# Kernel tuning notes

Measured on AMD Instinct MI355X. Metric: run time of the kernel, lower is better.

The kernel has to match this reference:

```python
import jax, jax.numpy as jnp
import numpy as np

D = 1024
NUM_HEADS = 16
HEAD_DIM = D // NUM_HEADS
INIT_VALUES = 1e-4


def setup_inputs() -> dict:
    key = jax.random.key(0)
    ks = jax.random.split(key, 24)
    s = 0.02
    inp = {
        "v": jax.random.normal(ks[0], (8, 2048, D), dtype=jnp.float32),
        "l": jax.random.normal(ks[1], (8, 512, D), dtype=jnp.float32),
        "ln_v_g": jnp.ones((D,), jnp.float32),
        "ln_v_b": jnp.zeros((D,), jnp.float32),
        "ln_l_g": jnp.ones((D,), jnp.float32),
        "ln_l_b": jnp.zeros((D,), jnp.float32),
        "gamma_v": jnp.full((D,), INIT_VALUES, jnp.float32),
        "gamma_l": jnp.full((D,), INIT_VALUES, jnp.float32),
    }
    names = ["Wq_v2l", "Wk_v2l", "Wv_v2l", "Wo_v2l", "Wq_l2v", "Wk_l2v", "Wv_l2v", "Wo_l2v"]
    for i, n in enumerate(names):
        inp[n] = jax.random.normal(ks[2 + i], (D, D), dtype=jnp.float32) * s
        inp[n.replace("W", "b")] = jnp.zeros((D,), jnp.float32)
    return inp


def layer_norm(x, g, b, eps=1e-5):
    mu = jnp.mean(x, axis=-1, keepdims=True)
    var = jnp.var(x, axis=-1, keepdims=True)
    return (x - mu) * jax.lax.rsqrt(var + eps) * g + b


def mha(q_in, k_in, v_in, Wq, bq, Wk, bk, Wv, bv, Wo, bo):
    B, Sq, _ = q_in.shape
    Sk = k_in.shape[1]
    # torch Linear: x @ W.T + b
    q = (q_in @ Wq.T + bq).reshape(B, Sq, NUM_HEADS, HEAD_DIM)
    k = (k_in @ Wk.T + bk).reshape(B, Sk, NUM_HEADS, HEAD_DIM)
    v = (v_in @ Wv.T + bv).reshape(B, Sk, NUM_HEADS, HEAD_DIM)
    scores = jnp.einsum("bqhd,bkhd->bhqk", q, k) / np.sqrt(HEAD_DIM).astype(np.float32)
    attn = jax.nn.softmax(scores, axis=-1)
    ctx = jnp.einsum("bhqk,bkhd->bqhd", attn, v).reshape(B, Sq, D)
    return ctx @ Wo.T + bo


def reference(v, l, ln_v_g, ln_v_b, ln_l_g, ln_l_b, gamma_v, gamma_l,
              Wq_v2l, bq_v2l, Wk_v2l, bk_v2l, Wv_v2l, bv_v2l, Wo_v2l, bo_v2l,
              Wq_l2v, bq_l2v, Wk_l2v, bk_l2v, Wv_l2v, bv_l2v, Wo_l2v, bo_l2v):
    # eval mode: dropout and drop_path are identity
    v_norm = layer_norm(v, ln_v_g, ln_v_b)
    l_norm = layer_norm(l, ln_l_g, ln_l_b)
    updated_v = mha(v_norm, l_norm, l_norm,
                    Wq_v2l, bq_v2l, Wk_v2l, bk_v2l, Wv_v2l, bv_v2l, Wo_v2l, bo_v2l)
    updated_l = mha(l_norm, v_norm, v_norm,
                    Wq_l2v, bq_l2v, Wk_l2v, bk_l2v, Wv_l2v, bv_l2v, Wo_l2v, bo_l2v)
    v_out = v + gamma_v * updated_v
    l_out = l + gamma_l * updated_l
    return (v_out, l_out)
```

## Files before the change

kernel.cpp:

```cpp
#include <hip/hip_runtime.h>
#include <hip/hip_bf16.h>
#include <stdint.h>

typedef __bf16 bf16x8 __attribute__((ext_vector_type(8)));
typedef float f32x4 __attribute__((ext_vector_type(4)));
typedef float f32x16 __attribute__((ext_vector_type(16)));
typedef uint32_t u32x4 __attribute__((ext_vector_type(4)));
typedef unsigned short u16;

typedef __attribute__((address_space(1))) void as1_void;
typedef __attribute__((address_space(3))) void as3_void;

#define BAR() __builtin_amdgcn_s_barrier()
#define VMCNT(n) asm volatile("s_waitcnt vmcnt(" #n ")" ::: "memory")
#define LGKM0() asm volatile("s_waitcnt lgkmcnt(0)" ::: "memory")

__device__ __forceinline__ u16 f2bf(float f) {
  uint32_t u = __float_as_uint(f);
  u += 0x7fffu + ((u >> 16) & 1u);
  return (u16)(u >> 16);
}

__device__ __forceinline__ uint32_t cvtpk(float lo, float hi) {
  uint32_t r;
  asm("v_cvt_pk_bf16_f32 %0, %1, %2" : "=v"(r) : "v"(lo), "v"(hi));
  return r;
}

__global__ __launch_bounds__(256) void cvt8_kernel(
    const float4* s0, const float4* s1, const float4* s2, const float4* s3,
    const float4* s4, const float4* s5, const float4* s6, const float4* s7,
    ushort4* d0, ushort4* d1, ushort4* d2, ushort4* d3,
    ushort4* d4, ushort4* d5, ushort4* d6, ushort4* d7) {
  const float4* s; ushort4* d;
  switch (blockIdx.y) {
    case 0: s = s0; d = d0; break;
    case 1: s = s1; d = d1; break;
    case 2: s = s2; d = d2; break;
    case 3: s = s3; d = d3; break;
    case 4: s = s4; d = d4; break;
    case 5: s = s5; d = d5; break;
    case 6: s = s6; d = d6; break;
    default: s = s7; d = d7; break;
  }
  int i = blockIdx.x * 256 + threadIdx.x;
  float4 v = s[i];
  ushort4 o;
  o.x = f2bf(v.x); o.y = f2bf(v.y); o.z = f2bf(v.z); o.w = f2bf(v.w);
  d[i] = o;
}

__global__ __launch_bounds__(256) void ln_kernel(const float* __restrict__ x,
                                                 const float* __restrict__ g,
                                                 const float* __restrict__ b,
                                                 u16* __restrict__ out) {
  int row = blockIdx.x;
  int t = threadIdx.x;
  const float4* xr = (const float4*)(x + (size_t)row * 1024);
  float4 v = xr[t];
  float s = v.x + v.y + v.z + v.w;
  float s2 = v.x * v.x + v.y * v.y + v.z * v.z + v.w * v.w;
#pragma unroll
  for (int off = 1; off < 64; off <<= 1) {
    s += __shfl_xor(s, off);
    s2 += __shfl_xor(s2, off);
  }
  __shared__ float red[8];
  int wv = t >> 6;
  if ((t & 63) == 0) { red[wv] = s; red[4 + wv] = s2; }
  __syncthreads();
  s = red[0] + red[1] + red[2] + red[3];
  s2 = red[4] + red[5] + red[6] + red[7];
  float mu = s * (1.0f / 1024.0f);
  float var = s2 * (1.0f / 1024.0f) - mu * mu;
  float rstd = rsqrtf(var + 1e-5f);
  const float4 gv = ((const float4*)g)[t];
  const float4 bv = ((const float4*)b)[t];
  ushort4 o;
  o.x = f2bf((v.x - mu) * rstd * gv.x + bv.x);
  o.y = f2bf((v.y - mu) * rstd * gv.y + bv.y);
  o.z = f2bf((v.z - mu) * rstd * gv.z + bv.z);
  o.w = f2bf((v.w - mu) * rstd * gv.w + bv.w);
  ((ushort4*)out)[(size_t)row * 256 + t] = o;
}

template <int MODE>
__global__ __launch_bounds__(256) void gemm_kernel(
    const u16* __restrict__ A, const u16* __restrict__ W,
    const float* __restrict__ bias,
    u16* __restrict__ outb, float* __restrict__ outf,
    const float* __restrict__ res, const float* __restrict__ gamma,
    int sk_shift, float ascale) {
  const int K = 1024, N = 1024;
  int m0 = blockIdx.x * 128, n0 = blockIdx.y * 128;
  int t = threadIdx.x, lane = t & 63, wv = t >> 6;
  int wr = wv >> 1, wc = wv & 1;
  int lr = lane & 15, lk = (lane >> 4) * 8;
  __shared__ u16 As[128 * 32];
  __shared__ u16 Ws[128 * 32];
  f32x4 acc[4][4] = {};
  for (int kt = 0; kt < K / 32; ++kt) {
#pragma unroll
    for (int i = 0; i < 2; ++i) {
      int c = i * 256 + t;
      int row = c >> 2, k8 = (c & 3) << 3;
      const u16* ga = A + (size_t)(m0 + row) * K + kt * 32 + k8;
      const u16* gw = W + (size_t)(n0 + row) * K + kt * 32 + k8;
      __builtin_amdgcn_global_load_lds((const as1_void*)ga, (as3_void*)(As + c * 8), 16, 0, 0);
      __builtin_amdgcn_global_load_lds((const as1_void*)gw, (as3_void*)(Ws + c * 8), 16, 0, 0);
    }
    __syncthreads();
    bf16x8 af[4], wf[4];
#pragma unroll
    for (int m = 0; m < 4; ++m)
      af[m] = *(const bf16x8*)(As + (wr * 64 + m * 16 + lr) * 32 + lk);
#pragma unroll
    for (int n = 0; n < 4; ++n)
      wf[n] = *(const bf16x8*)(Ws + (wc * 64 + n * 16 + lr) * 32 + lk);
#pragma unroll
    for (int m = 0; m < 4; ++m)
#pragma unroll
      for (int n = 0; n < 4; ++n)
        acc[m][n] = __builtin_amdgcn_mfma_f32_16x16x32_bf16(af[m], wf[n], acc[m][n], 0, 0, 0);
    __syncthreads();
  }
  int rowb = m0 + wr * 64 + (lane >> 4) * 4;
#pragma unroll
  for (int m = 0; m < 4; ++m) {
#pragma unroll
    for (int n = 0; n < 4; ++n) {
      int col = n0 + wc * 64 + n * 16 + lr;
      float bcol = bias[col];
#pragma unroll
      for (int r = 0; r < 4; ++r) {
        int row = rowb + m * 16 + r;
        float val = (acc[m][n][r] + bcol) * ascale;
        if (MODE == 0) {
          outb[(size_t)row * N + col] = f2bf(val);
        } else if (MODE == 1) {
          size_t idx = (size_t)row * N + col;
          outf[idx] = res[idx] + gamma[col] * val;
        } else {
          int bb = row >> sk_shift;
          int ss = row & ((1 << sk_shift) - 1);
          int h = col >> 6, d = col & 63;
          outb[((((size_t)bb * 16 + h) * 64 + d) << sk_shift) + ss] = f2bf(val);
        }
      }
    }
  }
}

template <int MODE>
__global__ __launch_bounds__(512, 2) void gemm256_kernel(
    const u16* __restrict__ A, const u16* __restrict__ W,
    const float* __restrict__ bias,
    u16* __restrict__ outb, float* __restrict__ outf,
    const float* __restrict__ res, const float* __restrict__ gamma,
    int mtiles, int sk_shift, float ascale) {
  const int K = 1024, N = 1024;
  int nwg = mtiles * 4;
  int cpx = nwg >> 3;
  int bid = blockIdx.x;
  int swz = (bid & 7) * cpx + (bid >> 3);
  int mt = swz >> 2, nt = swz & 3;
  int m0 = mt * 256, n0 = nt * 256;

  int t = threadIdx.x, lane = t & 63, wv = t >> 6;
  int wm = wv >> 2, wn = wv & 3;
  int lr = lane & 15, lg = lane >> 4;
  int sa0 = ((lg) ^ (lr & 7)) * 8;
  int sa1 = ((4 + lg) ^ (lr & 7)) * 8;

  __shared__ u16 AB[2][2][256 * 64];
  u16* ldsA0 = &AB[0][0][0];
  u16* ldsB0 = &AB[0][1][0];
  u16* ldsA1 = &AB[1][0][0];
  u16* ldsB1 = &AB[1][1][0];

  int r0 = t >> 3, c0 = t & 7;
  int cs0 = c0 ^ (r0 & 7);
  const u16* gA0 = A + (size_t)(m0 + r0) * K + cs0 * 8;
  const u16* gA1 = gA0 + (size_t)64 * K;
  const u16* gB0 = W + (size_t)(n0 + r0) * K + cs0 * 8;
  const u16* gB1 = gB0 + (size_t)64 * K;

  auto STG = [&](u16* ldsbase, const u16* g0, const u16* g1, int half, int kt) {
    __builtin_amdgcn_global_load_lds(
        (const as1_void*)(g0 + (size_t)half * 128 * K + kt * 64),
        (as3_void*)(ldsbase + (half * 128 + r0) * 64 + c0 * 8), 16, 0, 0);
    __builtin_amdgcn_global_load_lds(
        (const as1_void*)(g1 + (size_t)half * 128 * K + kt * 64),
        (as3_void*)(ldsbase + (half * 128 + r0 + 64) * 64 + c0 * 8), 16, 0, 0);
  };

  f32x4 acc[8][4] = {};
  bf16x8 aX[4][2], bX[2][2], bY[2][2];

  auto LD_A = [&](const u16* base, int mo) {
#pragma unroll
    for (int m = 0; m < 4; ++m) {
      const u16* rp = base + (wm * 128 + (mo + m) * 16 + lr) * 64;
      aX[m][0] = *(const bf16x8*)(rp + sa0);
      aX[m][1] = *(const bf16x8*)(rp + sa1);
    }
  };
  auto LD_B = [&](bf16x8 (&dst)[2][2], const u16* base, int no) {
#pragma unroll
    for (int n = 0; n < 2; ++n) {
      const u16* rp = base + (wn * 64 + (no + n) * 16 + lr) * 64;
      dst[n][0] = *(const bf16x8*)(rp + sa0);
      dst[n][1] = *(const bf16x8*)(rp + sa1);
    }
  };
  auto QD = [&](bf16x8 (&bf)[2][2], int mo, int no) {
#pragma unroll
    for (int m = 0; m < 4; ++m)
#pragma unroll
      for (int n = 0; n < 2; ++n) {
        acc[mo + m][no + n] = __builtin_amdgcn_mfma_f32_16x16x32_bf16(
            aX[m][0], bf[n][0], acc[mo + m][no + n], 0, 0, 0);
        acc[mo + m][no + n] = __builtin_amdgcn_mfma_f32_16x16x32_bf16(
            aX[m][1], bf[n][1], acc[mo + m][no + n], 0, 0, 0);
      }
  };

  STG(ldsA0, gA0, gA1, 0, 0); STG(ldsA0, gA0, gA1, 1, 0);
  STG(ldsB0, gB0, gB1, 0, 0); STG(ldsB0, gB0, gB1, 1, 0);
  STG(ldsA1, gA0, gA1, 0, 1); STG(ldsA1, gA0, gA1, 1, 1);
  STG(ldsB1, gB0, gB1, 0, 1); STG(ldsB1, gB0, gB1, 1, 1);
  VMCNT(8);
  BAR();

  const int NIT = K / 128;
#pragma unroll 1
  for (int it = 0; it < NIT; ++it) {
    bool st = (it + 1 < NIT);
    int ktA = 2 * it;
    LD_A(ldsA0, 0); LD_B(bX, ldsB0, 0);
    BAR(); LGKM0();
    __builtin_amdgcn_s_setprio(1); QD(bX, 0, 0); __builtin_amdgcn_s_setprio(0);
    BAR();
    LD_B(bY, ldsB0, 2);
    BAR(); LGKM0();
    __builtin_amdgcn_s_setprio(1); QD(bY, 0, 2); __builtin_amdgcn_s_setprio(0);
    BAR();
    LD_A(ldsA0, 4);
    if (st) { STG(ldsB0, gB0, gB1, 0, ktA + 2); STG(ldsB0, gB0, gB1, 1, ktA + 2); }
    BAR(); LGKM0();
    __builtin_amdgcn_s_setprio(1); QD(bY, 4, 2); __builtin_amdgcn_s_setprio(0);
    BAR();
    if (st) { STG(ldsA0, gA0, gA1, 0, ktA + 2); STG(ldsA0, gA0, gA1, 1, ktA + 2); }
    if (st) { VMCNT(8); } else { VMCNT(0); }
    BAR();
    __builtin_amdgcn_s_setprio(1); QD(bX, 4, 0); __builtin_amdgcn_s_setprio(0);
    BAR();
    LD_A(ldsA1, 0); LD_B(bX, ldsB1, 0);
    BAR(); LGKM0();
    __builtin_amdgcn_s_setprio(1); QD(bX, 0, 0); __builtin_amdgcn_s_setprio(0);
    BAR();
    LD_B(bY, ldsB1, 2);
    BAR(); LGKM0();
    __builtin_amdgcn_s_setprio(1); QD(bY, 0, 2); __builtin_amdgcn_s_setprio(0);
    BAR();
    LD_A(ldsA1, 4);
    if (st) { STG(ldsB1, gB0, gB1, 0, ktA + 3); STG(ldsB1, gB0, gB1, 1, ktA + 3); }
    BAR(); LGKM0();
    __builtin_amdgcn_s_setprio(1); QD(bY, 4, 2); __builtin_amdgcn_s_setprio(0);
    BAR();
    if (st) { STG(ldsA1, gA0, gA1, 0, ktA + 3); STG(ldsA1, gA0, gA1, 1, ktA + 3); }
    if (st) { VMCNT(8); }
    BAR();
    __builtin_amdgcn_s_setprio(1); QD(bX, 4, 0); __builtin_amdgcn_s_setprio(0);
    BAR();
  }

  int rowb = m0 + wm * 128 + lg * 4;
#pragma unroll
  for (int mi = 0; mi < 8; ++mi) {
#pragma unroll
    for (int n = 0; n < 4; ++n) {
      int col = n0 + wn * 64 + n * 16 + lr;
      float bcol = bias[col];
#pragma unroll
      for (int r = 0; r < 4; ++r) {
        int row = rowb + mi * 16 + r;
        float val = (acc[mi][n][r] + bcol) * ascale;
        if (MODE == 0) {
          outb[(size_t)row * N + col] = f2bf(val);
        } else if (MODE == 1) {
          size_t idx = (size_t)row * N + col;
          outf[idx] = res[idx] + gamma[col] * val;
        } else {
          int bb = row >> sk_shift;
          int ss = row & ((1 << sk_shift) - 1);
          int h = col >> 6, d = col & 63;
          outb[((((size_t)bb * 16 + h) * 64 + d) << sk_shift) + ss] = f2bf(val);
        }
      }
    }
  }
}

__global__ __launch_bounds__(256, 4) void attn_kernel(
    const u16* __restrict__ Q, const u16* __restrict__ Kmat,
    const u16* __restrict__ Vt, u16* __restrict__ ctx,
    int Sq, int Sk, int nq_shift) {
  int f = blockIdx.x;
  int xcd = f & 7, slot = f >> 3;
  int group = xcd * 16 + (slot >> nq_shift);
  int qt = slot & ((1 << nq_shift) - 1);
  int b = group >> 4, h = group & 15;
  int t = threadIdx.x, lane = t & 63, wv = t >> 6;
  int l31 = lane & 31, hi = lane >> 5;

  __shared__ u16 Ks[2][64 * 64];
  __shared__ u16 Vs[2][64 * 64];

  int q0 = qt * 128 + wv * 32;
  const u16* Qb = Q + (size_t)(b * Sq + q0 + l31) * 1024 + h * 64 + hi * 8;
  bf16x8 qf[4];
#pragma unroll
  for (int ds = 0; ds < 4; ++ds) qf[ds] = *(const bf16x8*)(Qb + ds * 16);

  int trow = t >> 3, tc = t & 7;
  int sc = (tc ^ (trow & 7)) * 8;
  const u16* gk = Kmat + (size_t)(b * Sk + trow) * 1024 + h * 64 + sc;
  const u16* gv = Vt + (size_t)((b * 16 + h) * 64 + trow) * Sk + sc;

  auto STAGE = [&](int buf, int kt) {
    const u16* k0 = gk + (size_t)(kt * 64) * 1024;
    const u16* v0 = gv + kt * 64;
    __builtin_amdgcn_global_load_lds((const as1_void*)k0, (as3_void*)(Ks[buf] + t * 8), 16, 0, 0);
    __builtin_amdgcn_global_load_lds((const as1_void*)(k0 + (size_t)32 * 1024), (as3_void*)(Ks[buf] + 2048 + t * 8), 16, 0, 0);
    __builtin_amdgcn_global_load_lds((const as1_void*)v0, (as3_void*)(Vs[buf] + t * 8), 16, 0, 0);
    __builtin_amdgcn_global_load_lds((const as1_void*)(v0 + (size_t)32 * Sk), (as3_void*)(Vs[buf] + 2048 + t * 8), 16, 0, 0);
  };

  STAGE(0, 0);
  __syncthreads();

  f32x16 acc0 = {}, acc1 = {};
  float m_run = -1e30f, l_run = 0.f;
  int sw = l31 & 7;

  int nt = Sk >> 6;
  for (int kt = 0; kt < nt; ++kt) {
    int cur = kt & 1;
    if (kt + 1 < nt) STAGE(cur ^ 1, kt + 1);
    const u16* kb = Ks[cur];
    f32x16 s0v = {}, s1v = {};
    __builtin_amdgcn_s_setprio(1);
#pragma unroll
    for (int ds = 0; ds < 4; ++ds) {
      int blk = 2 * ds + hi;
      bf16x8 ka0 = *(const bf16x8*)(kb + l31 * 64 + ((blk ^ sw) * 8));
      bf16x8 ka1 = *(const bf16x8*)(kb + (32 + l31) * 64 + ((blk ^ sw) * 8));
      s0v = __builtin_amdgcn_mfma_f32_32x32x16_bf16(ka0, qf[ds], s0v, 0, 0, 0);
      s1v = __builtin_amdgcn_mfma_f32_32x32x16_bf16(ka1, qf[ds], s1v, 0, 0, 0);
    }
    __builtin_amdgcn_s_setprio(0);
    float mx = s0v[0];
#pragma unroll
    for (int i = 1; i < 16; ++i) mx = fmaxf(mx, s0v[i]);
#pragma unroll
    for (int i = 0; i < 16; ++i) mx = fmaxf(mx, s1v[i]);
    mx = fmaxf(mx, __shfl_xor(mx, 32));
    if (__any(mx > m_run + 8.f)) {
      float mnew = fmaxf(m_run, mx);
      float fac = __builtin_amdgcn_exp2f(m_run - mnew);
#pragma unroll
      for (int r = 0; r < 16; ++r) {
        int src = (r & 3) + 8 * (r >> 2) + 4 * hi;
        float fr = __shfl(fac, src);
        acc0[r] *= fr;
        acc1[r] *= fr;
      }
      l_run *= fac;
      m_run = mnew;
    }
    float sum = 0.f;
#pragma unroll
    for (int i = 0; i < 16; ++i) {
      s0v[i] = __builtin_amdgcn_exp2f(s0v[i] - m_run);
      sum += s0v[i];
    }
#pragma unroll
    for (int i = 0; i < 16; ++i) {
      s1v[i] = __builtin_amdgcn_exp2f(s1v[i] - m_run);
      sum += s1v[i];
    }
    sum += __shfl_xor(sum, 32);
    l_run += sum;
    bf16x8 pa[4];
#pragma unroll
    for (int g = 0; g < 2; ++g) {
      const f32x16& s = g ? s1v : s0v;
#pragma unroll
      for (int half = 0; half < 2; ++half) {
        int o = half * 8;
        uint32_t a0 = cvtpk(s[o + 0], s[o + 1]);
        uint32_t a1 = cvtpk(s[o + 2], s[o + 3]);
        uint32_t b0 = cvtpk(s[o + 4], s[o + 5]);
        uint32_t b1 = cvtpk(s[o + 6], s[o + 7]);
        asm("v_permlane32_swap_b32 %0, %1" : "+v"(a0), "+v"(b0));
        asm("v_permlane32_swap_b32 %0, %1" : "+v"(a1), "+v"(b1));
        u32x4 w;
        w[0] = a0; w[1] = a1; w[2] = b0; w[3] = b1;
        pa[g * 2 + half] = __builtin_bit_cast(bf16x8, w);
      }
    }
    const u16* vb = Vs[cur];
    __builtin_amdgcn_s_setprio(1);
#pragma unroll
    for (int ks = 0; ks < 4; ++ks) {
      int blk = 2 * ks + hi;
      bf16x8 vf0 = *(const bf16x8*)(vb + l31 * 64 + ((blk ^ sw) * 8));
      bf16x8 vf1 = *(const bf16x8*)(vb + (32 + l31) * 64 + ((blk ^ sw) * 8));
      acc0 = __builtin_amdgcn_mfma_f32_32x32x16_bf16(pa[ks], vf0, acc0, 0, 0, 0);
      acc1 = __builtin_amdgcn_mfma_f32_32x32x16_bf16(pa[ks], vf1, acc1, 0, 0, 0);
    }
    __builtin_amdgcn_s_setprio(0);
    __syncthreads();
  }
  float linv = 1.0f / l_run;
  u16* cb = ctx + (size_t)(b * Sq + q0) * 1024 + h * 64;
#pragma unroll
  for (int r = 0; r < 16; ++r) {
    int src = (r & 3) + 8 * (r >> 2) + 4 * hi;
    float li = __shfl(linv, src);
    cb[(size_t)src * 1024 + l31] = f2bf(acc0[r] * li);
    cb[(size_t)src * 1024 + 32 + l31] = f2bf(acc1[r] * li);
  }
}

extern "C" void kernel_launch(void* const* d_in, const int* in_sizes, int n_in,
                              void* d_out, int out_size, void* d_ws, size_t ws_size,
                              hipStream_t stream) {
  const float* v = (const float*)d_in[0];
  const float* l = (const float*)d_in[1];
  const float* ln_v_g = (const float*)d_in[2];
  const float* ln_v_b = (const float*)d_in[3];
  const float* ln_l_g = (const float*)d_in[4];
  const float* ln_l_b = (const float*)d_in[5];
  const float* gamma_v = (const float*)d_in[6];
  const float* gamma_l = (const float*)d_in[7];
  const float* Wf[8];
  const float* Bf[8];
  for (int i = 0; i < 8; ++i) {
    Wf[i] = (const float*)d_in[8 + 2 * i];
    Bf[i] = (const float*)d_in[9 + 2 * i];
  }
  float* v_out = (float*)d_out;
  float* l_out = v_out + (size_t)16384 * 1024;

  char* p = (char*)d_ws;
  auto alloc = [&](size_t bytes) {
    char* r = p;
    p += (bytes + 255) & ~(size_t)255;
    return r;
  };
  u16* Wbf[8];
  for (int i = 0; i < 8; ++i) Wbf[i] = (u16*)alloc((size_t)1024 * 1024 * 2);
  u16* vn   = (u16*)alloc((size_t)16384 * 1024 * 2);
  u16* lnm  = (u16*)alloc((size_t)4096 * 1024 * 2);
  u16* bufA = (u16*)alloc((size_t)16384 * 1024 * 2);
  u16* bufB = (u16*)alloc((size_t)4096 * 1024 * 2);
  u16* bufC = (u16*)alloc((size_t)4096 * 1024 * 2);
  u16* bufD = (u16*)alloc((size_t)16384 * 1024 * 2);

  const float QSC = 0.125f * 1.4426950408889634f;

  cvt8_kernel<<<dim3(1024, 8), 256, 0, stream>>>(
      (const float4*)Wf[0], (const float4*)Wf[1], (const float4*)Wf[2], (const float4*)Wf[3],
      (const float4*)Wf[4], (const float4*)Wf[5], (const float4*)Wf[6], (const float4*)Wf[7],
      (ushort4*)Wbf[0], (ushort4*)Wbf[1], (ushort4*)Wbf[2], (ushort4*)Wbf[3],
      (ushort4*)Wbf[4], (ushort4*)Wbf[5], (ushort4*)Wbf[6], (ushort4*)Wbf[7]);
  ln_kernel<<<16384, 256, 0, stream>>>(v, ln_v_g, ln_v_b, vn);
  ln_kernel<<<4096, 256, 0, stream>>>(l, ln_l_g, ln_l_b, lnm);

  dim3 blk(256);
  dim3 blk512(512);
  gemm256_kernel<0><<<dim3(256), blk512, 0, stream>>>(vn, Wbf[0], Bf[0], bufA, nullptr, nullptr, nullptr, 64, 0, QSC);
  gemm_kernel<0><<<dim3(32, 8), blk, 0, stream>>>(lnm, Wbf[1], Bf[1], bufB, nullptr, nullptr, nullptr, 0, 1.0f);
  gemm_kernel<2><<<dim3(32, 8), blk, 0, stream>>>(lnm, Wbf[2], Bf[2], bufC, nullptr, nullptr, nullptr, 9, 1.0f);
  attn_kernel<<<dim3(2048), blk, 0, stream>>>(bufA, bufB, bufC, bufD, 2048, 512, 4);
  gemm256_kernel<1><<<dim3(256), blk512, 0, stream>>>(bufD, Wbf[3], Bf[3], nullptr, v_out, v, gamma_v, 64, 0, 1.0f);
  gemm_kernel<0><<<dim3(32, 8), blk, 0, stream>>>(lnm, Wbf[4], Bf[4], bufB, nullptr, nullptr, nullptr, 0, QSC);
  gemm256_kernel<0><<<dim3(256), blk512, 0, stream>>>(vn, Wbf[5], Bf[5], bufA, nullptr, nullptr, nullptr, 64, 0, 1.0f);
  gemm256_kernel<2><<<dim3(256), blk512, 0, stream>>>(vn, Wbf[6], Bf[6], bufD, nullptr, nullptr, nullptr, 64, 11, 1.0f);
  attn_kernel<<<dim3(512), blk, 0, stream>>>(bufB, bufA, bufD, bufC, 512, 2048, 2);
  gemm_kernel<1><<<dim3(32, 8), blk, 0, stream>>>(bufC, Wbf[7], Bf[7], nullptr, l_out, l, gamma_l, 0, 1.0f);
}
```

Baseline: 435.0 us.

## Replace GEMM kernels with unified triple-buffered 128-tile GEMM and fuse same-input projections

Both earlier GEMM kernels are replaced by one 128x128 GEMM with a 3-stage global_load_lds pipeline, XOR-swizzled LDS and XCD-aware block mapping. Projections that share the same input (Q/K/V from l_norm, and K/V from v_norm) are batched into single launches through a segment descriptor, which cuts launch count and reuses the A tiles across segments. The attention output now overwrites its Q buffer in place. In exchange, the large-M GEMMs lose the 256x256 tile and its higher arithmetic intensity, and the epilogue now branches on a runtime mode.

```diff
diff --git a/kernel.cpp b/kernel.cpp
--- a/kernel.cpp
+++ b/kernel.cpp
@@ -21,11 +21,17 @@
   return (u16)(u >> 16);
 }
 
-__device__ __forceinline__ uint32_t cvtpk(float lo, float hi) {
-  uint32_t r;
-  asm("v_cvt_pk_bf16_f32 %0, %1, %2" : "=v"(r) : "v"(lo), "v"(hi));
-  return r;
-}
+struct Seg {
+  const u16* W;
+  const float* bias;
+  u16* outb;
+  float* outf;
+  const float* res;
+  const float* gamma;
+  int mode;
+  int sk;
+  float ascale;
+};
 
 __global__ __launch_bounds__(256) void cvt8_kernel(
     const float4* s0, const float4* s1, const float4* s2, const float4* s3,
@@ -84,218 +90,102 @@
   ((ushort4*)out)[(size_t)row * 256 + t] = o;
 }
 
-template <int MODE>
-__global__ __launch_bounds__(256) void gemm_kernel(
-    const u16* __restrict__ A, const u16* __restrict__ W,
-    const float* __restrict__ bias,
-    u16* __restrict__ outb, float* __restrict__ outf,
-    const float* __restrict__ res, const float* __restrict__ gamma,
-    int sk_shift, float ascale) {
-  const int K = 1024, N = 1024;
-  int m0 = blockIdx.x * 128, n0 = blockIdx.y * 128;
+__global__ __launch_bounds__(256, 3) void gemm_v7(
+    const u16* __restrict__ A, Seg s0, Seg s1, Seg s2,
+    int mtiles, int ntiles) {
+  const int K = 1024;
+  int hwid = blockIdx.x;
+  int xcd = hwid & 7, q = hwid >> 3;
+  int mchunk = mtiles >> 3;
+  int mt = xcd * mchunk + q / ntiles;
+  int nt = q % ntiles;
+  int m0 = mt * 128;
+  int si = nt >> 3;
+  Seg seg = (si == 0) ? s0 : (si == 1) ? s1 : s2;
+  int nl0 = (nt & 7) * 128;
+
   int t = threadIdx.x, lane = t & 63, wv = t >> 6;
   int wr = wv >> 1, wc = wv & 1;
-  int lr = lane & 15, lk = (lane >> 4) * 8;
-  __shared__ u16 As[128 * 32];
-  __shared__ u16 Ws[128 * 32];
+  int lr = lane & 15, lg = lane >> 4;
+
+  __shared__ u16 SA[3][128 * 32];
+  __shared__ u16 SB[3][128 * 32];
+
+  int row0 = t >> 2, c0 = t & 3;
+  int sco = (c0 ^ (row0 & 3)) * 8;
+  const u16* gA0 = A + (size_t)(m0 + row0) * K + sco;
+  const u16* gB0 = seg.W + (size_t)(nl0 + row0) * K + sco;
+
+  auto STAGE = [&](int slot, int kt) {
+    __builtin_amdgcn_global_load_lds((const as1_void*)(gA0 + kt * 32),
+                                     (as3_void*)(&SA[slot][0] + t * 8), 16, 0, 0);
+    __builtin_amdgcn_global_load_lds((const as1_void*)(gA0 + (size_t)64 * K + kt * 32),
+                                     (as3_void*)(&SA[slot][0] + 2048 + t * 8), 16, 0, 0);
+    __builtin_amdgcn_global_load_lds((const as1_void*)(gB0 + kt * 32),
+                                     (as3_void*)(&SB[slot][0] + t * 8), 16, 0, 0);
+    __builtin_amdgcn_global_load_lds((const as1_void*)(gB0 + (size_t)64 * K + kt * 32),
+                                     (as3_void*)(&SB[slot][0] + 2048 + t * 8), 16, 0, 0);
+  };
+
   f32x4 acc[4][4] = {};
-  for (int kt = 0; kt < K / 32; ++kt) {
-#pragma unroll
-    for (int i = 0; i < 2; ++i) {
-      int c = i * 256 + t;
-      int row = c >> 2, k8 = (c & 3) << 3;
-      const u16* ga = A + (size_t)(m0 + row) * K + kt * 32 + k8;
-      const u16* gw = W + (size_t)(n0 + row) * K + kt * 32 + k8;
-      __builtin_amdgcn_global_load_lds((const as1_void*)ga, (as3_void*)(As + c * 8), 16, 0, 0);
-      __builtin_amdgcn_global_load_lds((const as1_void*)gw, (as3_void*)(Ws + c * 8), 16, 0, 0);
-    }
-    __syncthreads();
-    bf16x8 af[4], wf[4];
+
+  STAGE(0, 0); STAGE(1, 1); STAGE(2, 2);
+  VMCNT(8);
+  BAR();
+
+  int slot = 0;
+  const int NKT = K / 32;
+#pragma unroll 1
+  for (int kt = 0; kt < NKT; ++kt) {
+    bf16x8 aX[4], bX[4];
+#pragma unroll
+    for (int m = 0; m < 4; ++m) {
+      int row = wr * 64 + m * 16 + lr;
+      aX[m] = *(const bf16x8*)(&SA[slot][0] + row * 32 + ((lg ^ (row & 3)) * 8));
+    }
+#pragma unroll
+    for (int n = 0; n < 4; ++n) {
+      int row = wc * 64 + n * 16 + lr;
+      bX[n] = *(const bf16x8*)(&SB[slot][0] + row * 32 + ((lg ^ (row & 3)) * 8));
+    }
+    LGKM0();
+    BAR();
+    if (kt + 3 < NKT) STAGE(slot, kt + 3);
+    __builtin_amdgcn_s_setprio(1);
 #pragma unroll
     for (int m = 0; m < 4; ++m)
-      af[m] = *(const bf16x8*)(As + (wr * 64 + m * 16 + lr) * 32 + lk);
-#pragma unroll
-    for (int n = 0; n < 4; ++n)
-      wf[n] = *(const bf16x8*)(Ws + (wc * 64 + n * 16 + lr) * 32 + lk);
-#pragma unroll
-    for (int m = 0; m < 4; ++m)
 #pragma unroll
       for (int n = 0; n < 4; ++n)
-        acc[m][n] = __builtin_amdgcn_mfma_f32_16x16x32_bf16(af[m], wf[n], acc[m][n], 0, 0, 0);
-    __syncthreads();
-  }
+        acc[m][n] = __builtin_amdgcn_mfma_f32_16x16x32_bf16(aX[m], bX[n], acc[m][n], 0, 0, 0);
+    __builtin_amdgcn_s_setprio(0);
+    if (kt + 3 < NKT) { VMCNT(8); }
+    else if (kt + 3 == NKT) { VMCNT(4); }
+    else if (kt + 2 == NKT) { VMCNT(0); }
+    BAR();
+    slot = (slot == 2) ? 0 : slot + 1;
+  }
+
   int rowb = m0 + wr * 64 + (lane >> 4) * 4;
 #pragma unroll
   for (int m = 0; m < 4; ++m) {
 #pragma unroll
     for (int n = 0; n < 4; ++n) {
-      int col = n0 + wc * 64 + n * 16 + lr;
-      float bcol = bias[col];
+      int scol = nl0 + wc * 64 + n * 16 + lr;
+      float bcol = seg.bias[scol];
 #pragma unroll
       for (int r = 0; r < 4; ++r) {
         int row = rowb + m * 16 + r;
-        float val = (acc[m][n][r] + bcol) * ascale;
-        if (MODE == 0) {
-          outb[(size_t)row * N + col] = f2bf(val);
-        } else if (MODE == 1) {
-          size_t idx = (size_t)row * N + col;
-          outf[idx] = res[idx] + gamma[col] * val;
+        float val = (acc[m][n][r] + bcol) * seg.ascale;
+        if (seg.mode == 0) {
+          seg.outb[(size_t)row * 1024 + scol] = f2bf(val);
+        } else if (seg.mode == 1) {
+          size_t idx = (size_t)row * 1024 + scol;
+          seg.outf[idx] = seg.res[idx] + seg.gamma[scol] * val;
         } else {
-          int bb = row >> sk_shift;
-          int ss = row & ((1 << sk_shift) - 1);
-          int h = col >> 6, d = col & 63;
-          outb[((((size_t)bb * 16 + h) * 64 + d) << sk_shift) + ss] = f2bf(val);
-        }
-      }
-    }
-  }
-}
-
-template <int MODE>
-__global__ __launch_bounds__(512, 2) void gemm256_kernel(
-    const u16* __restrict__ A, const u16* __restrict__ W,
-    const float* __restrict__ bias,
-    u16* __restrict__ outb, float* __restrict__ outf,
-    const float* __restrict__ res, const float* __restrict__ gamma,
-    int mtiles, int sk_shift, float ascale) {
-  const int K = 1024, N = 1024;
-  int nwg = mtiles * 4;
-  int cpx = nwg >> 3;
-  int bid = blockIdx.x;
-  int swz = (bid & 7) * cpx + (bid >> 3);
-  int mt = swz >> 2, nt = swz & 3;
-  int m0 = mt * 256, n0 = nt * 256;
-
-  int t = threadIdx.x, lane = t & 63, wv = t >> 6;
-  int wm = wv >> 2, wn = wv & 3;
-  int lr = lane & 15, lg = lane >> 4;
-  int sa0 = ((lg) ^ (lr & 7)) * 8;
-  int sa1 = ((4 + lg) ^ (lr & 7)) * 8;
-
-  __shared__ u16 AB[2][2][256 * 64];
-  u16* ldsA0 = &AB[0][0][0];
-  u16* ldsB0 = &AB[0][1][0];
-  u16* ldsA1 = &AB[1][0][0];
-  u16* ldsB1 = &AB[1][1][0];
-
-  int r0 = t >> 3, c0 = t & 7;
-  int cs0 = c0 ^ (r0 & 7);
-  const u16* gA0 = A + (size_t)(m0 + r0) * K + cs0 * 8;
-  const u16* gA1 = gA0 + (size_t)64 * K;
-  const u16* gB0 = W + (size_t)(n0 + r0) * K + cs0 * 8;
-  const u16* gB1 = gB0 + (size_t)64 * K;
-
-  auto STG = [&](u16* ldsbase, const u16* g0, const u16* g1, int half, int kt) {
-    __builtin_amdgcn_global_load_lds(
-        (const as1_void*)(g0 + (size_t)half * 128 * K + kt * 64),
-        (as3_void*)(ldsbase + (half * 128 + r0) * 64 + c0 * 8), 16, 0, 0);
-    __builtin_amdgcn_global_load_lds(
-        (const as1_void*)(g1 + (size_t)half * 128 * K + kt * 64),
-        (as3_void*)(ldsbase + (half * 128 + r0 + 64) * 64 + c0 * 8), 16, 0, 0);
-  };
-
-  f32x4 acc[8][4] = {};
-  bf16x8 aX[4][2], bX[2][2], bY[2][2];
-
-  auto LD_A = [&](const u16* base, int mo) {
-#pragma unroll
-    for (int m = 0; m < 4; ++m) {
-      const u16* rp = base + (wm * 128 + (mo + m) * 16 + lr) * 64;
-      aX[m][0] = *(const bf16x8*)(rp + sa0);
-      aX[m][1] = *(const bf16x8*)(rp + sa1);
-    }
-  };
-  auto LD_B = [&](bf16x8 (&dst)[2][2], const u16* base, int no) {
-#pragma unroll
-    for (int n = 0; n < 2; ++n) {
-      const u16* rp = base + (wn * 64 + (no + n) * 16 + lr) * 64;
-      dst[n][0] = *(const bf16x8*)(rp + sa0);
-      dst[n][1] = *(const bf16x8*)(rp + sa1);
-    }
-  };
-  auto QD = [&](bf16x8 (&bf)[2][2], int mo, int no) {
-#pragma unroll
-    for (int m = 0; m < 4; ++m)
-#pragma unroll
-      for (int n = 0; n < 2; ++n) {
-        acc[mo + m][no + n] = __builtin_amdgcn_mfma_f32_16x16x32_bf16(
-            aX[m][0], bf[n][0], acc[mo + m][no + n], 0, 0, 0);
-        acc[mo + m][no + n] = __builtin_amdgcn_mfma_f32_16x16x32_bf16(
-            aX[m][1], bf[n][1], acc[mo + m][no + n], 0, 0, 0);
-      }
-  };
-
-  STG(ldsA0, gA0, gA1, 0, 0); STG(ldsA0, gA0, gA1, 1, 0);
-  STG(ldsB0, gB0, gB1, 0, 0); STG(ldsB0, gB0, gB1, 1, 0);
-  STG(ldsA1, gA0, gA1, 0, 1); STG(ldsA1, gA0, gA1, 1, 1);
-  STG(ldsB1, gB0, gB1, 0, 1); STG(ldsB1, gB0, gB1, 1, 1);
-  VMCNT(8);
-  BAR();
-
-  const int NIT = K / 128;
-#pragma unroll 1
-  for (int it = 0; it < NIT; ++it) {
-    bool st = (it + 1 < NIT);
-    int ktA = 2 * it;
-    LD_A(ldsA0, 0); LD_B(bX, ldsB0, 0);
-    BAR(); LGKM0();
-    __builtin_amdgcn_s_setprio(1); QD(bX, 0, 0); __builtin_amdgcn_s_setprio(0);
-    BAR();
-    LD_B(bY, ldsB0, 2);
-    BAR(); LGKM0();
-    __builtin_amdgcn_s_setprio(1); QD(bY, 0, 2); __builtin_amdgcn_s_setprio(0);
-    BAR();
-    LD_A(ldsA0, 4);
-    if (st) { STG(ldsB0, gB0, gB1, 0, ktA + 2); STG(ldsB0, gB0, gB1, 1, ktA + 2); }
-    BAR(); LGKM0();
-    __builtin_amdgcn_s_setprio(1); QD(bY, 4, 2); __builtin_amdgcn_s_setprio(0);
-    BAR();
-    if (st) { STG(ldsA0, gA0, gA1, 0, ktA + 2); STG(ldsA0, gA0, gA1, 1, ktA + 2); }
-    if (st) { VMCNT(8); } else { VMCNT(0); }
-    BAR();
-    __builtin_amdgcn_s_setprio(1); QD(bX, 4, 0); __builtin_amdgcn_s_setprio(0);
-    BAR();
-    LD_A(ldsA1, 0); LD_B(bX, ldsB1, 0);
-    BAR(); LGKM0();
-    __builtin_amdgcn_s_setprio(1); QD(bX, 0, 0); __builtin_amdgcn_s_setprio(0);
-    BAR();
-    LD_B(bY, ldsB1, 2);
-    BAR(); LGKM0();
-    __builtin_amdgcn_s_setprio(1); QD(bY, 0, 2); __builtin_amdgcn_s_setprio(0);
-    BAR();
-    LD_A(ldsA1, 4);
-    if (st) { STG(ldsB1, gB0, gB1, 0, ktA + 3); STG(ldsB1, gB0, gB1, 1, ktA + 3); }
-    BAR(); LGKM0();
-    __builtin_amdgcn_s_setprio(1); QD(bY, 4, 2); __builtin_amdgcn_s_setprio(0);
-    BAR();
-    if (st) { STG(ldsA1, gA0, gA1, 0, ktA + 3); STG(ldsA1, gA0, gA1, 1, ktA + 3); }
-    if (st) { VMCNT(8); }
-    BAR();
-    __builtin_amdgcn_s_setprio(1); QD(bX, 4, 0); __builtin_amdgcn_s_setprio(0);
-    BAR();
-  }
-
-  int rowb = m0 + wm * 128 + lg * 4;
-#pragma unroll
-  for (int mi = 0; mi < 8; ++mi) {
-#pragma unroll
-    for (int n = 0; n < 4; ++n) {
-      int col = n0 + wn * 64 + n * 16 + lr;
-      float bcol = bias[col];
-#pragma unroll
-      for (int r = 0; r < 4; ++r) {
-        int row = rowb + mi * 16 + r;
-        float val = (acc[mi][n][r] + bcol) * ascale;
-        if (MODE == 0) {
-          outb[(size_t)row * N + col] = f2bf(val);
-        } else if (MODE == 1) {
-          size_t idx = (size_t)row * N + col;
-          outf[idx] = res[idx] + gamma[col] * val;
-        } else {
-          int bb = row >> sk_shift;
-          int ss = row & ((1 << sk_shift) - 1);
-          int h = col >> 6, d = col & 63;
-          outb[((((size_t)bb * 16 + h) * 64 + d) << sk_shift) + ss] = f2bf(val);
+          int bb = row >> seg.sk;
+          int ss = row & ((1 << seg.sk) - 1);
+          int h = scol >> 6, d = scol & 63;
+          seg.outb[((((size_t)bb * 16 + h) * 64 + d) << seg.sk) + ss] = f2bf(val);
         }
       }
     }
@@ -399,10 +289,11 @@
 #pragma unroll
       for (int half = 0; half < 2; ++half) {
         int o = half * 8;
-        uint32_t a0 = cvtpk(s[o + 0], s[o + 1]);
-        uint32_t a1 = cvtpk(s[o + 2], s[o + 3]);
-        uint32_t b0 = cvtpk(s[o + 4], s[o + 5]);
-        uint32_t b1 = cvtpk(s[o + 6], s[o + 7]);
+        uint32_t a0, a1, b0, b1;
+        asm("v_cvt_pk_bf16_f32 %0, %1, %2" : "=v"(a0) : "v"(s[o + 0]), "v"(s[o + 1]));
+        asm("v_cvt_pk_bf16_f32 %0, %1, %2" : "=v"(a1) : "v"(s[o + 2]), "v"(s[o + 3]));
+        asm("v_cvt_pk_bf16_f32 %0, %1, %2" : "=v"(b0) : "v"(s[o + 4]), "v"(s[o + 5]));
+        asm("v_cvt_pk_bf16_f32 %0, %1, %2" : "=v"(b1) : "v"(s[o + 6]), "v"(s[o + 7]));
         asm("v_permlane32_swap_b32 %0, %1" : "+v"(a0), "+v"(b0));
         asm("v_permlane32_swap_b32 %0, %1" : "+v"(a1), "+v"(b1));
         u32x4 w;
@@ -468,8 +359,10 @@
   u16* bufB = (u16*)alloc((size_t)4096 * 1024 * 2);
   u16* bufC = (u16*)alloc((size_t)4096 * 1024 * 2);
   u16* bufD = (u16*)alloc((size_t)16384 * 1024 * 2);
+  u16* bufF = (u16*)alloc((size_t)4096 * 1024 * 2);
 
   const float QSC = 0.125f * 1.4426950408889634f;
+  Seg zs = {};
 
   cvt8_kernel<<<dim3(1024, 8), 256, 0, stream>>>(
       (const float4*)Wf[0], (const float4*)Wf[1], (const float4*)Wf[2], (const float4*)Wf[3],
@@ -479,16 +372,29 @@
   ln_kernel<<<16384, 256, 0, stream>>>(v, ln_v_g, ln_v_b, vn);
   ln_kernel<<<4096, 256, 0, stream>>>(l, ln_l_g, ln_l_b, lnm);
 
-  dim3 blk(256);
-  dim3 blk512(512);
-  gemm256_kernel<0><<<dim3(256), blk512, 0, stream>>>(vn, Wbf[0], Bf[0], bufA, nullptr, nullptr, nullptr, 64, 0, QSC);
-  gemm_kernel<0><<<dim3(32, 8), blk, 0, stream>>>(lnm, Wbf[1], Bf[1], bufB, nullptr, nullptr, nullptr, 0, 1.0f);
-  gemm_kernel<2><<<dim3(32, 8), blk, 0, stream>>>(lnm, Wbf[2], Bf[2], bufC, nullptr, nullptr, nullptr, 9, 1.0f);
-  attn_kernel<<<dim3(2048), blk, 0, stream>>>(bufA, bufB, bufC, bufD, 2048, 512, 4);
-  gemm256_kernel<1><<<dim3(256), blk512, 0, stream>>>(bufD, Wbf[3], Bf[3], nullptr, v_out, v, gamma_v, 64, 0, 1.0f);
-  gemm_kernel<0><<<dim3(32, 8), blk, 0, stream>>>(lnm, Wbf[4], Bf[4], bufB, nullptr, nullptr, nullptr, 0, QSC);
-  gemm256_kernel<0><<<dim3(256), blk512, 0, stream>>>(vn, Wbf[5], Bf[5], bufA, nullptr, nullptr, nullptr, 64, 0, 1.0f);
-  gemm256_kernel<2><<<dim3(256), blk512, 0, stream>>>(vn, Wbf[6], Bf[6], bufD, nullptr, nullptr, nullptr, 64, 11, 1.0f);
-  attn_kernel<<<dim3(512), blk, 0, stream>>>(bufB, bufA, bufD, bufC, 512, 2048, 2);
-  gemm_kernel<1><<<dim3(32, 8), blk, 0, stream>>>(bufC, Wbf[7], Bf[7], nullptr, l_out, l, gamma_l, 0, 1.0f);
-}
+  {
+    Seg a = {Wbf[4], Bf[4], bufB, nullptr, nullptr, nullptr, 0, 0, QSC};
+    Seg b = {Wbf[1], Bf[1], bufF, nullptr, nullptr, nullptr, 0, 0, 1.0f};
+    Seg c = {Wbf[2], Bf[2], bufC, nullptr, nullptr, nullptr, 2, 9, 1.0f};
+    gemm_v7<<<dim3(768), 256, 0, stream>>>(lnm, a, b, c, 32, 24);
+  }
+  {
+    Seg q = {Wbf[0], Bf[0], bufA, nullptr, nullptr, nullptr, 0, 0, QSC};
+    gemm_v7<<<dim3(1024), 256, 0, stream>>>(vn, q, zs, zs, 128, 8);
+  }
+  attn_kernel<<<dim3(2048), 256, 0, stream>>>(bufA, bufF, bufC, bufA, 2048, 512, 4);
+  {
+    Seg o = {Wbf[3], Bf[3], nullptr, v_out, v, gamma_v, 1, 0, 1.0f};
+    gemm_v7<<<dim3(1024), 256, 0, stream>>>(bufA, o, zs, zs, 128, 8);
+  }
+  {
+    Seg k = {Wbf[5], Bf[5], bufA, nullptr, nullptr, nullptr, 0, 0, 1.0f};
+    Seg vv = {Wbf[6], Bf[6], bufD, nullptr, nullptr, nullptr, 2, 11, 1.0f};
+    gemm_v7<<<dim3(2048), 256, 0, stream>>>(vn, k, vv, zs, 128, 16);
+  }
+  attn_kernel<<<dim3(512), 256, 0, stream>>>(bufB, bufA, bufD, bufB, 512, 2048, 2);
+  {
+    Seg o = {Wbf[7], Bf[7], nullptr, l_out, l, gamma_l, 1, 0, 1.0f};
+    gemm_v7<<<dim3(256), 256, 0, stream>>>(bufB, o, zs, zs, 32, 8);
+  }
+}
```

New measurement: 506.3 us. 16.4% more time.
